# Kernel tuning notes

Measured on AMD Instinct MI355X. Metric: run time of the kernel, lower is better.

Reference implementation:

```python
import jax, jax.numpy as jnp
import numpy as np

N_EXPERTS = 8
DIM = 2048
INTER = 1408
TOTAL_TOKENS = 16384
ALPHA = 1.702
LIMIT = 7.0
LINEAR_OFFSET = 1.0


def setup_inputs() -> dict:
    key = jax.random.key(0)
    k1, k2, k3, k4 = jax.random.split(key, 4)
    x = jax.random.normal(k1, (TOTAL_TOKENS, DIM), dtype=jnp.float32)
    permuted_probs = jax.random.uniform(k2, (TOTAL_TOKENS, 1), dtype=jnp.float32)
    # Stacked-transposed views as in gate_and_up_projs / down_projs properties:
    # [E, in_features, out_features]
    gate_up_w = jax.random.normal(k3, (N_EXPERTS, DIM, 2 * INTER), dtype=jnp.float32) * (DIM ** -0.5)
    down_w = jax.random.normal(k4, (N_EXPERTS, INTER, DIM), dtype=jnp.float32) * (INTER ** -0.5)
    tokens_per_expert = jnp.full((N_EXPERTS,), TOTAL_TOKENS // N_EXPERTS, dtype=jnp.int32)
    return {"x": x, "permuted_probs": permuted_probs, "gate_up_w": gate_up_w,
            "down_w": down_w, "tokens_per_expert": tokens_per_expert}


def quick_geglu(h, probs):
    # interleaved split, as x[..., ::2] / x[..., 1::2]
    gate = jnp.minimum(h[..., ::2], LIMIT)
    up = jnp.clip(h[..., 1::2], -LIMIT, LIMIT)
    glu = gate * jax.nn.sigmoid(ALPHA * gate)
    inter = glu * (up + LINEAR_OFFSET)
    return (inter * probs).astype(h.dtype)


def reference(x, permuted_probs, gate_up_w, down_w, tokens_per_expert):
    # tokens are pre-permuted: equal static group sizes per expert (fp8 pad/unpad
    # is an identity on the math; grouped GEMM expressed as batched einsum).
    E = gate_up_w.shape[0]
    xr = x.reshape(E, -1, DIM)                      # [E, T, dim]
    h = jnp.einsum('etd,edf->etf', xr, gate_up_w)   # [E, T, 2*inter]
    probs = permuted_probs.reshape(E, -1, 1)
    act = quick_geglu(h, probs)                     # [E, T, inter]
    out = jnp.einsum('eti,eio->eto', act, down_w)   # [E, T, dim]
    return out.reshape(-1, DIM)
```

## Files before the change

### kernel.cpp

```cpp
#include <hip/hip_runtime.h>
#include <hip/hip_bf16.h>
#include <stdint.h>

#define N_EXPERTS 8
#define DIM 2048
#define INTER 1408
#define NGU (2*INTER)
#define TOK_E 2048
#define TOTAL_TOKENS 16384

typedef __attribute__((ext_vector_type(8))) short short8;
typedef __attribute__((ext_vector_type(4))) float f32x4;

__device__ __forceinline__ unsigned short f2bf(float f) {
    union { float f; unsigned u; } v; v.f = f;
    unsigned r = v.u + 0x7FFF + ((v.u >> 16) & 1);
    return (unsigned short)(r >> 16);
}

#define GLOAD16(G, L) __builtin_amdgcn_global_load_lds( \
    (const __attribute__((address_space(1))) void*)(G), \
    (__attribute__((address_space(3))) void*)(L), 16, 0, 0)


__global__ void convert_x(const float* __restrict__ in, unsigned short* __restrict__ out, int n8) {
    int i = blockIdx.x * blockDim.x + threadIdx.x;
    int stride = gridDim.x * blockDim.x;
    for (; i < n8; i += stride) {
        const float4* p = (const float4*)(in + (size_t)i * 8);
        float4 v0 = p[0], v1 = p[1];
        union { unsigned short u[8]; uint4 q; } o;
        o.u[0]=f2bf(v0.x); o.u[1]=f2bf(v0.y); o.u[2]=f2bf(v0.z); o.u[3]=f2bf(v0.w);
        o.u[4]=f2bf(v1.x); o.u[5]=f2bf(v1.y); o.u[6]=f2bf(v1.z); o.u[7]=f2bf(v1.w);
        *(uint4*)(out + (size_t)i * 8) = o.q;
    }
}

__global__ __launch_bounds__(256)
void transpose_convert(const float* __restrict__ in, unsigned short* __restrict__ out,
                       int K, int N, int permute) {
    __shared__ float tile[32][129];
    const int n0 = blockIdx.x * 32, k0 = blockIdx.y * 128;
    const size_t ein  = (size_t)blockIdx.z * K * N;
    const size_t eout = (size_t)blockIdx.z * N * K;
    const int tc = threadIdx.x & 31;
    const int tr = threadIdx.x >> 5;
    #pragma unroll
    for (int i = 0; i < 16; ++i) {
        int k = tr + i * 8;
        tile[tc][k] = in[ein + (size_t)(k0 + k) * N + n0 + tc];
    }
    __syncthreads();
    const int kg = threadIdx.x & 31;
    const int r0 = threadIdx.x >> 5;
    #pragma unroll
    for (int i = 0; i < 4; ++i) {
        int r = r0 + i * 8;
        int c = n0 + r;
        int dr = c;
        if (permute) {
            int a = c >> 1;
            dr = ((a >> 4) << 5) + (a & 15) + ((c & 1) << 4);
        }
        union { unsigned short u[4]; uint2 q; } o;
        #pragma unroll
        for (int j = 0; j < 4; ++j) o.u[j] = f2bf(tile[r][kg * 4 + j]);
        *(uint2*)(out + eout + (size_t)dr * K + k0 + kg * 4) = o.q;
    }
}


#define SB0 __builtin_amdgcn_sched_barrier(0)
#define VMC(N_) asm volatile("s_waitcnt vmcnt(" #N_ ")" ::: "memory")
#define LGK8 asm volatile("s_waitcnt lgkmcnt(8)" ::: "memory")

#define GEMM_PROLOG(LDKC) \
    const int t = threadIdx.x; \
    const int lane = t & 63, wid = t >> 6; \
    const int wm = wid >> 2, wn = wid & 3;             \
    const int l15 = lane & 15; \
    const int rd0 = (lane & 15) * 64 + (((lane >> 4) ^ (lane & 7)) * 8); \
    const int rd1 = (lane & 15) * 64 + ((((lane >> 4) + 4) ^ (lane & 7)) * 8); \
    const size_t goff = (size_t)(t >> 3) * (LDKC) + (size_t)(((t & 7) ^ ((t >> 3) & 7)) * 8); \
    const int ldsw = wid * 512 + lane * 8;

#define STGA(LDKC, bb_, h_, kt_) do { \
    const unsigned short* g_ = gA + (size_t)(h_) * 128 * (LDKC) + (size_t)(kt_) * 64 + goff; \
    unsigned short* l_ = sA + (bb_) * 16384 + (h_) * 8192 + ldsw; \
    GLOAD16(g_, l_); GLOAD16(g_ + (size_t)64 * (LDKC), l_ + 4096); \
} while (0)

#define STGB(LDKC, bb_, h_, kt_) do { \
    const unsigned short* g_ = gB + (size_t)(h_) * 128 * (LDKC) + (size_t)(kt_) * 64 + goff; \
    unsigned short* l_ = sB + (bb_) * 16384 + (h_) * 8192 + ldsw; \
    GLOAD16(g_, l_); GLOAD16(g_ + (size_t)64 * (LDKC), l_ + 4096); \
} while (0)

#define DSA2(bb_, qm_) do { \
    const unsigned short* p_ = &sA[(bb_) * 16384 + ((qm_) * 128 + wm * 64) * 64]; \
    _Pragma("unroll") for (int m_ = 0; m_ < 4; ++m_) { \
        a[m_][0] = *(const short8*)(p_ + m_ * 1024 + rd0); \
        a[m_][1] = *(const short8*)(p_ + m_ * 1024 + rd1); } \
} while (0)

#define DSB2(bb_, qn_, R_) do { \
    const unsigned short* p_ = &sB[(bb_) * 16384 + ((qn_) * 128 + wn * 32) * 64]; \
    _Pragma("unroll") for (int n_ = 0; n_ < 2; ++n_) { \
        R_[n_][0] = *(const short8*)(p_ + n_ * 1024 + rd0); \
        R_[n_][1] = *(const short8*)(p_ + n_ * 1024 + rd1); } \
} while (0)

#define QMF(qm_, qn_, B_) do { \
    _Pragma("unroll") for (int m_ = 0; m_ < 4; ++m_) { \
        _Pragma("unroll") for (int n_ = 0; n_ < 2; ++n_) { \
            acc[qm_][qn_][m_][n_] = __builtin_amdgcn_mfma_f32_16x16x32_bf16(a[m_][0], B_[n_][0], acc[qm_][qn_][m_][n_], 0, 0, 0); \
            acc[qm_][qn_][m_][n_] = __builtin_amdgcn_mfma_f32_16x16x32_bf16(a[m_][1], B_[n_][1], acc[qm_][qn_][m_][n_], 0, 0, 0); \
        } } \
} while (0)

#define PH(DSOPS, STGOPS, MFOPS, ENDOPS) do { \
    DSOPS; \
    STGOPS; \
    SB0; \
    __builtin_amdgcn_s_barrier(); \
    asm volatile("s_waitcnt lgkmcnt(0)" ::: "memory"); \
    SB0; \
    __builtin_amdgcn_s_setprio(1); \
    MFOPS; \
    __builtin_amdgcn_s_setprio(0); \
    SB0; \
    ENDOPS; \
    __builtin_amdgcn_s_barrier(); \
} while (0)

#define ITER8(LDKC, kt0_, SG2, SG3, SG4, SG5, SG6, SG7, SG8, E4, E8) \
    PH(DSA2(0,0); DSB2(0,0,bq0); LGK8, STGA(LDKC,1,1,(kt0_)+1), QMF(0,0,bq0), ); \
    PH(DSB2(0,1,bq1),            SG2,                     QMF(0,1,bq1), ); \
    PH(DSA2(0,1),                SG3,                     QMF(1,0,bq0), ); \
    PH(,                         SG4,                     QMF(1,1,bq1), E4); \
    PH(DSA2(1,0); DSB2(1,0,bq0); LGK8, SG5,               QMF(0,0,bq0), ); \
    PH(DSB2(1,1,bq1),            SG6,                     QMF(0,1,bq1), ); \
    PH(DSA2(1,1),                SG7,                     QMF(1,0,bq0), ); \
    PH(,                         SG8,                     QMF(1,1,bq1), E8);

#define GEMM_PIPE(LDKC, NI_) \
    short8 a[4][2], bq0[2][2], bq1[2][2]; \
    f32x4 acc[2][2][4][2]; \
    _Pragma("unroll") for (int q_ = 0; q_ < 2; ++q_) \
    _Pragma("unroll") for (int r_ = 0; r_ < 2; ++r_) \
    _Pragma("unroll") for (int m_ = 0; m_ < 4; ++m_) \
    _Pragma("unroll") for (int n_ = 0; n_ < 2; ++n_) acc[q_][r_][m_][n_] = (f32x4)0.0f; \
     \
    STGA(LDKC,0,0,0); STGB(LDKC,0,0,0); STGB(LDKC,0,1,0); STGA(LDKC,0,1,0); \
    STGA(LDKC,1,0,1); STGB(LDKC,1,0,1); STGB(LDKC,1,1,1); \
    VMC(6); \
    __builtin_amdgcn_s_barrier(); \
    for (int it = 0; it < (NI_) - 1; ++it) { \
        const int kt0 = 2 * it; \
        ITER8(LDKC, kt0, \
              STGA(LDKC,0,0,kt0+2), STGB(LDKC,0,0,kt0+2), STGB(LDKC,0,1,kt0+2), STGA(LDKC,0,1,kt0+2), \
              STGA(LDKC,1,0,kt0+3), STGB(LDKC,1,0,kt0+3), STGB(LDKC,1,1,kt0+3), \
              VMC(6), VMC(6)) \
    } \
    { \
        const int kt0 = 2 * ((NI_) - 1); \
        ITER8(LDKC, kt0, , , , , , , , VMC(0), ) \
    }


__global__ __launch_bounds__(512, 2)
void gemm_gu(const unsigned short* __restrict__ A,
             const unsigned short* __restrict__ Bt,
             const float* __restrict__ probs,
             unsigned short* __restrict__ act) {
    __shared__ unsigned short sA[2 * 16384];
    __shared__ unsigned short sB[2 * 16384];
    GEMM_PROLOG(DIM)
    const int bid = blockIdx.x;
    const int e = bid & 7;
    const int local = bid >> 3;
    const int tm = local & 7;
    const int tn = local >> 3;
    const unsigned short* gA = A  + (size_t)(e * TOK_E + tm * 256) * DIM;
    const unsigned short* gB = Bt + (size_t)e * NGU * DIM + (size_t)(tn * 256) * DIM;

    GEMM_PIPE(DIM, 16)

    const int rgrp = lane >> 4;
    #pragma unroll
    for (int qm = 0; qm < 2; ++qm) {
        #pragma unroll
        for (int qn = 0; qn < 2; ++qn) {
            const int acol = tn * 128 + qn * 64 + wn * 16 + l15;
            #pragma unroll
            for (int m = 0; m < 4; ++m) {
                const int row0 = e * TOK_E + tm * 256 + qm * 128 + wm * 64 + m * 16 + rgrp * 4;
                #pragma unroll
                for (int j = 0; j < 4; ++j) {
                    float p = probs[row0 + j];
                    float g = fminf(acc[qm][qn][m][0][j], 7.0f);
                    float u = fminf(fmaxf(acc[qm][qn][m][1][j], -7.0f), 7.0f);
                    float glu = g / (1.0f + __expf(-1.702f * g));
                    float r = glu * (u + 1.0f) * p;
                    act[(size_t)(row0 + j) * INTER + acol] = f2bf(r);
                }
            }
        }
    }
}


__global__ __launch_bounds__(512, 2)
void gemm_down(const unsigned short* __restrict__ A,
               const unsigned short* __restrict__ Bt,
               float* __restrict__ out) {
    __shared__ unsigned short sA[2 * 16384];
    __shared__ unsigned short sB[2 * 16384];
    GEMM_PROLOG(INTER)
    const int bid = blockIdx.x;
    const int e = bid & 7;
    const int local = bid >> 3;
    const int tm = local & 7;
    const int tn = local >> 3;
    const unsigned short* gA = A  + (size_t)(e * TOK_E + tm * 256) * INTER;
    const unsigned short* gB = Bt + (size_t)e * DIM * INTER + (size_t)(tn * 256) * INTER;

    GEMM_PIPE(INTER, 11)

    const int rgrp = lane >> 4;
    #pragma unroll
    for (int qm = 0; qm < 2; ++qm) {
        #pragma unroll
        for (int qn = 0; qn < 2; ++qn) {
            #pragma unroll
            for (int m = 0; m < 4; ++m) {
                const int row0 = e * TOK_E + tm * 256 + qm * 128 + wm * 64 + m * 16 + rgrp * 4;
                #pragma unroll
                for (int j = 0; j < 4; ++j) {
                    #pragma unroll
                    for (int n = 0; n < 2; ++n) {
                        const int col = tn * 256 + qn * 128 + wn * 32 + n * 16 + l15;
                        out[(size_t)(row0 + j) * DIM + col] = acc[qm][qn][m][n][j];
                    }
                }
            }
        }
    }
}


extern "C" void kernel_launch(void* const* d_in, const int* in_sizes, int n_in,
                              void* d_out, int out_size, void* d_ws, size_t ws_size,
                              hipStream_t stream) {
    const float* x     = (const float*)d_in[0];
    const float* probs = (const float*)d_in[1];
    const float* gup   = (const float*)d_in[2];
    const float* dwn   = (const float*)d_in[3];
    float* out = (float*)d_out;

    char* ws = (char*)d_ws;
    const size_t SZ_XB  = (size_t)TOTAL_TOKENS * DIM * 2;
    const size_t SZ_GUB = (size_t)N_EXPERTS * NGU * DIM * 2;
    const size_t SZ_DWB = (size_t)N_EXPERTS * DIM * INTER * 2;
    unsigned short* xb   = (unsigned short*)(ws);
    unsigned short* gub  = (unsigned short*)(ws + SZ_XB);
    unsigned short* dwb  = (unsigned short*)(ws + SZ_XB + SZ_GUB);
    unsigned short* actb = (unsigned short*)(ws + SZ_XB + SZ_GUB + SZ_DWB);

    convert_x<<<2048, 256, 0, stream>>>(x, xb, TOTAL_TOKENS * DIM / 8);

    dim3 tg1(NGU / 32, DIM / 128, N_EXPERTS);
    transpose_convert<<<tg1, 256, 0, stream>>>(gup, gub, DIM, NGU, 1);
    dim3 tg2(DIM / 32, INTER / 128, N_EXPERTS);
    transpose_convert<<<tg2, 256, 0, stream>>>(dwn, dwb, INTER, DIM, 0);

    gemm_gu<<<704, 512, 0, stream>>>(xb, gub, probs, actb);
    gemm_down<<<512, 512, 0, stream>>>(actb, dwb, out);
}
```

Baseline: 407.6 us.

## Fuse the prep conversion kernels into one launch and drop explicit LDS waits

```diff
diff --git a/kernel.cpp b/kernel.cpp
--- a/kernel.cpp
+++ b/kernel.cpp
@@ -22,27 +22,46 @@
     (const __attribute__((address_space(1))) void*)(G), \
     (__attribute__((address_space(3))) void*)(L), 16, 0, 0)
 
-
-__global__ void convert_x(const float* __restrict__ in, unsigned short* __restrict__ out, int n8) {
-    int i = blockIdx.x * blockDim.x + threadIdx.x;
-    int stride = gridDim.x * blockDim.x;
-    for (; i < n8; i += stride) {
-        const float4* p = (const float4*)(in + (size_t)i * 8);
-        float4 v0 = p[0], v1 = p[1];
-        union { unsigned short u[8]; uint4 q; } o;
-        o.u[0]=f2bf(v0.x); o.u[1]=f2bf(v0.y); o.u[2]=f2bf(v0.z); o.u[3]=f2bf(v0.w);
-        o.u[4]=f2bf(v1.x); o.u[5]=f2bf(v1.y); o.u[6]=f2bf(v1.z); o.u[7]=f2bf(v1.w);
-        *(uint4*)(out + (size_t)i * 8) = o.q;
-    }
-}
+#define NB_CONV 2048
+#define NB_GUP  (88 * 16 * 8)
+#define NB_DWN  (64 * 11 * 8)
 
 __global__ __launch_bounds__(256)
-void transpose_convert(const float* __restrict__ in, unsigned short* __restrict__ out,
-                       int K, int N, int permute) {
+void prep_fused(const float* __restrict__ x, unsigned short* __restrict__ xb,
+                const float* __restrict__ gup, unsigned short* __restrict__ gub,
+                const float* __restrict__ dwn, unsigned short* __restrict__ dwb) {
     __shared__ float tile[32][129];
-    const int n0 = blockIdx.x * 32, k0 = blockIdx.y * 128;
-    const size_t ein  = (size_t)blockIdx.z * K * N;
-    const size_t eout = (size_t)blockIdx.z * N * K;
+    const int b = blockIdx.x;
+    if (b < NB_CONV) {
+        const int n8 = TOTAL_TOKENS * DIM / 8;
+        int i = b * 256 + threadIdx.x;
+        const int stride = NB_CONV * 256;
+        for (; i < n8; i += stride) {
+            const float4* p = (const float4*)(x + (size_t)i * 8);
+            float4 v0 = p[0], v1 = p[1];
+            union { unsigned short u[8]; uint4 q; } o;
+            o.u[0]=f2bf(v0.x); o.u[1]=f2bf(v0.y); o.u[2]=f2bf(v0.z); o.u[3]=f2bf(v0.w);
+            o.u[4]=f2bf(v1.x); o.u[5]=f2bf(v1.y); o.u[6]=f2bf(v1.z); o.u[7]=f2bf(v1.w);
+            *(uint4*)(xb + (size_t)i * 8) = o.q;
+        }
+        return;
+    }
+    const float* in; unsigned short* out; int K, N, permute, local, nbx;
+    if (b < NB_CONV + NB_GUP) {
+        in = gup; out = gub; K = DIM; N = NGU; permute = 1;
+        local = b - NB_CONV; nbx = NGU / 32;
+    } else {
+        in = dwn; out = dwb; K = INTER; N = DIM; permute = 0;
+        local = b - NB_CONV - NB_GUP; nbx = DIM / 32;
+    }
+    const int bx = local % nbx;
+    const int rem = local / nbx;
+    const int nby = K / 128;
+    const int by = rem % nby;
+    const int bz = rem / nby;
+    const int n0 = bx * 32, k0 = by * 128;
+    const size_t ein  = (size_t)bz * K * N;
+    const size_t eout = (size_t)bz * N * K;
     const int tc = threadIdx.x & 31;
     const int tr = threadIdx.x >> 5;
     #pragma unroll
@@ -72,7 +91,6 @@
 
 #define SB0 __builtin_amdgcn_sched_barrier(0)
 #define VMC(N_) asm volatile("s_waitcnt vmcnt(" #N_ ")" ::: "memory")
-#define LGK8 asm volatile("s_waitcnt lgkmcnt(8)" ::: "memory")
 
 #define GEMM_PROLOG(LDKC) \
     const int t = threadIdx.x; \
@@ -123,8 +141,6 @@
     STGOPS; \
     SB0; \
     __builtin_amdgcn_s_barrier(); \
-    asm volatile("s_waitcnt lgkmcnt(0)" ::: "memory"); \
-    SB0; \
     __builtin_amdgcn_s_setprio(1); \
     MFOPS; \
     __builtin_amdgcn_s_setprio(0); \
@@ -134,11 +150,11 @@
 } while (0)
 
 #define ITER8(LDKC, kt0_, SG2, SG3, SG4, SG5, SG6, SG7, SG8, E4, E8) \
-    PH(DSA2(0,0); DSB2(0,0,bq0); LGK8, STGA(LDKC,1,1,(kt0_)+1), QMF(0,0,bq0), ); \
+    PH(DSA2(0,0); DSB2(0,0,bq0), STGA(LDKC,1,1,(kt0_)+1), QMF(0,0,bq0), ); \
     PH(DSB2(0,1,bq1),            SG2,                     QMF(0,1,bq1), ); \
     PH(DSA2(0,1),                SG3,                     QMF(1,0,bq0), ); \
     PH(,                         SG4,                     QMF(1,1,bq1), E4); \
-    PH(DSA2(1,0); DSB2(1,0,bq0); LGK8, SG5,               QMF(0,0,bq0), ); \
+    PH(DSA2(1,0); DSB2(1,0,bq0), SG5,                     QMF(0,0,bq0), ); \
     PH(DSB2(1,1,bq1),            SG6,                     QMF(0,1,bq1), ); \
     PH(DSA2(1,1),                SG7,                     QMF(1,0,bq0), ); \
     PH(,                         SG8,                     QMF(1,1,bq1), E8);
@@ -267,12 +283,7 @@
     unsigned short* dwb  = (unsigned short*)(ws + SZ_XB + SZ_GUB);
     unsigned short* actb = (unsigned short*)(ws + SZ_XB + SZ_GUB + SZ_DWB);
 
-    convert_x<<<2048, 256, 0, stream>>>(x, xb, TOTAL_TOKENS * DIM / 8);
-
-    dim3 tg1(NGU / 32, DIM / 128, N_EXPERTS);
-    transpose_convert<<<tg1, 256, 0, stream>>>(gup, gub, DIM, NGU, 1);
-    dim3 tg2(DIM / 32, INTER / 128, N_EXPERTS);
-    transpose_convert<<<tg2, 256, 0, stream>>>(dwn, dwb, INTER, DIM, 0);
+    prep_fused<<<NB_CONV + NB_GUP + NB_DWN, 256, 0, stream>>>(x, xb, gup, gub, dwn, dwb);
 
     gemm_gu<<<704, 512, 0, stream>>>(xb, gub, probs, actb);
     gemm_down<<<512, 512, 0, stream>>>(actb, dwb, out);
```

Measured after the change: 426.9 us. +4.7%, slower.

## Switch GEMMs to 32x32x16 MFMA with matching weight permutation and LDS reads

Applied to the files above, without the earlier changes.

```diff
diff --git a/kernel.cpp b/kernel.cpp
--- a/kernel.cpp
+++ b/kernel.cpp
@@ -10,7 +10,7 @@
 #define TOTAL_TOKENS 16384
 
 typedef __attribute__((ext_vector_type(8))) short short8;
-typedef __attribute__((ext_vector_type(4))) float f32x4;
+typedef __attribute__((ext_vector_type(16))) float f32x16;
 
 __device__ __forceinline__ unsigned short f2bf(float f) {
     union { float f; unsigned u; } v; v.f = f;
@@ -60,7 +60,7 @@
         int dr = c;
         if (permute) {
             int a = c >> 1;
-            dr = ((a >> 4) << 5) + (a & 15) + ((c & 1) << 4);
+            dr = ((a >> 5) << 6) + (a & 31) + ((c & 1) << 5);
         }
         union { unsigned short u[4]; uint2 q; } o;
         #pragma unroll
@@ -78,9 +78,11 @@
     const int t = threadIdx.x; \
     const int lane = t & 63, wid = t >> 6; \
     const int wm = wid >> 2, wn = wid & 3;             \
-    const int l15 = lane & 15; \
-    const int rd0 = (lane & 15) * 64 + (((lane >> 4) ^ (lane & 7)) * 8); \
-    const int rd1 = (lane & 15) * 64 + ((((lane >> 4) + 4) ^ (lane & 7)) * 8); \
+    const int row31 = lane & 31, h5 = lane >> 5; \
+    const int so0 = ((0 * 2 + h5) ^ (lane & 7)) * 8; \
+    const int so1 = ((1 * 2 + h5) ^ (lane & 7)) * 8; \
+    const int so2 = ((2 * 2 + h5) ^ (lane & 7)) * 8; \
+    const int so3 = ((3 * 2 + h5) ^ (lane & 7)) * 8; \
     const size_t goff = (size_t)(t >> 3) * (LDKC) + (size_t)(((t & 7) ^ ((t >> 3) & 7)) * 8); \
     const int ldsw = wid * 512 + lane * 8;
 
@@ -97,24 +99,23 @@
 } while (0)
 
 #define DSA2(bb_, qm_) do { \
-    const unsigned short* p_ = &sA[(bb_) * 16384 + ((qm_) * 128 + wm * 64) * 64]; \
-    _Pragma("unroll") for (int m_ = 0; m_ < 4; ++m_) { \
-        a[m_][0] = *(const short8*)(p_ + m_ * 1024 + rd0); \
-        a[m_][1] = *(const short8*)(p_ + m_ * 1024 + rd1); } \
+    const unsigned short* p_ = &sA[(bb_) * 16384 + ((qm_) * 128 + wm * 64 + row31) * 64]; \
+    a[0][0] = *(const short8*)(p_ + so0);        a[0][1] = *(const short8*)(p_ + so1); \
+    a[0][2] = *(const short8*)(p_ + so2);        a[0][3] = *(const short8*)(p_ + so3); \
+    a[1][0] = *(const short8*)(p_ + 2048 + so0); a[1][1] = *(const short8*)(p_ + 2048 + so1); \
+    a[1][2] = *(const short8*)(p_ + 2048 + so2); a[1][3] = *(const short8*)(p_ + 2048 + so3); \
 } while (0)
 
 #define DSB2(bb_, qn_, R_) do { \
-    const unsigned short* p_ = &sB[(bb_) * 16384 + ((qn_) * 128 + wn * 32) * 64]; \
-    _Pragma("unroll") for (int n_ = 0; n_ < 2; ++n_) { \
-        R_[n_][0] = *(const short8*)(p_ + n_ * 1024 + rd0); \
-        R_[n_][1] = *(const short8*)(p_ + n_ * 1024 + rd1); } \
+    const unsigned short* p_ = &sB[(bb_) * 16384 + (wn * 64 + (qn_) * 32 + row31) * 64]; \
+    R_[0] = *(const short8*)(p_ + so0); R_[1] = *(const short8*)(p_ + so1); \
+    R_[2] = *(const short8*)(p_ + so2); R_[3] = *(const short8*)(p_ + so3); \
 } while (0)
 
 #define QMF(qm_, qn_, B_) do { \
-    _Pragma("unroll") for (int m_ = 0; m_ < 4; ++m_) { \
-        _Pragma("unroll") for (int n_ = 0; n_ < 2; ++n_) { \
-            acc[qm_][qn_][m_][n_] = __builtin_amdgcn_mfma_f32_16x16x32_bf16(a[m_][0], B_[n_][0], acc[qm_][qn_][m_][n_], 0, 0, 0); \
-            acc[qm_][qn_][m_][n_] = __builtin_amdgcn_mfma_f32_16x16x32_bf16(a[m_][1], B_[n_][1], acc[qm_][qn_][m_][n_], 0, 0, 0); \
+    _Pragma("unroll") for (int s_ = 0; s_ < 4; ++s_) { \
+        _Pragma("unroll") for (int m_ = 0; m_ < 2; ++m_) { \
+            acc[qm_][qn_][m_] = __builtin_amdgcn_mfma_f32_32x32x16_bf16(a[m_][s_], B_[s_], acc[qm_][qn_][m_], 0, 0, 0); \
         } } \
 } while (0)
 
@@ -122,15 +123,14 @@
     DSOPS; \
     STGOPS; \
     SB0; \
+    asm volatile("s_waitcnt lgkmcnt(0)" ::: "memory"); \
+    ENDOPS; \
+    SB0; \
     __builtin_amdgcn_s_barrier(); \
-    asm volatile("s_waitcnt lgkmcnt(0)" ::: "memory"); \
-    SB0; \
     __builtin_amdgcn_s_setprio(1); \
     MFOPS; \
     __builtin_amdgcn_s_setprio(0); \
     SB0; \
-    ENDOPS; \
-    __builtin_amdgcn_s_barrier(); \
 } while (0)
 
 #define ITER8(LDKC, kt0_, SG2, SG3, SG4, SG5, SG6, SG7, SG8, E4, E8) \
@@ -144,12 +144,11 @@
     PH(,                         SG8,                     QMF(1,1,bq1), E8);
 
 #define GEMM_PIPE(LDKC, NI_) \
-    short8 a[4][2], bq0[2][2], bq1[2][2]; \
-    f32x4 acc[2][2][4][2]; \
+    short8 a[2][4], bq0[4], bq1[4]; \
+    f32x16 acc[2][2][2]; \
     _Pragma("unroll") for (int q_ = 0; q_ < 2; ++q_) \
     _Pragma("unroll") for (int r_ = 0; r_ < 2; ++r_) \
-    _Pragma("unroll") for (int m_ = 0; m_ < 4; ++m_) \
-    _Pragma("unroll") for (int n_ = 0; n_ < 2; ++n_) acc[q_][r_][m_][n_] = (f32x4)0.0f; \
+    _Pragma("unroll") for (int m_ = 0; m_ < 2; ++m_) acc[q_][r_][m_] = (f32x16)0.0f; \
      \
     STGA(LDKC,0,0,0); STGB(LDKC,0,0,0); STGB(LDKC,0,1,0); STGA(LDKC,0,1,0); \
     STGA(LDKC,1,0,1); STGB(LDKC,1,0,1); STGB(LDKC,1,1,1); \
@@ -186,24 +185,21 @@
 
     GEMM_PIPE(DIM, 16)
 
-    const int rgrp = lane >> 4;
+    const int acol = tn * 128 + wn * 32 + row31;
     #pragma unroll
     for (int qm = 0; qm < 2; ++qm) {
         #pragma unroll
-        for (int qn = 0; qn < 2; ++qn) {
-            const int acol = tn * 128 + qn * 64 + wn * 16 + l15;
+        for (int m = 0; m < 2; ++m) {
+            const int rbase = e * TOK_E + tm * 256 + qm * 128 + wm * 64 + m * 32 + 4 * h5;
             #pragma unroll
-            for (int m = 0; m < 4; ++m) {
-                const int row0 = e * TOK_E + tm * 256 + qm * 128 + wm * 64 + m * 16 + rgrp * 4;
-                #pragma unroll
-                for (int j = 0; j < 4; ++j) {
-                    float p = probs[row0 + j];
-                    float g = fminf(acc[qm][qn][m][0][j], 7.0f);
-                    float u = fminf(fmaxf(acc[qm][qn][m][1][j], -7.0f), 7.0f);
-                    float glu = g / (1.0f + __expf(-1.702f * g));
-                    float r = glu * (u + 1.0f) * p;
-                    act[(size_t)(row0 + j) * INTER + acol] = f2bf(r);
-                }
+            for (int r = 0; r < 16; ++r) {
+                const int row = rbase + (r & 3) + 8 * (r >> 2);
+                float p = probs[row];
+                float g = fminf(acc[qm][0][m][r], 7.0f);
+                float u = fminf(fmaxf(acc[qm][1][m][r], -7.0f), 7.0f);
+                float glu = g / (1.0f + __expf(-1.702f * g));
+                float rv = glu * (u + 1.0f) * p;
+                act[(size_t)row * INTER + acol] = f2bf(rv);
             }
         }
     }
@@ -227,21 +223,18 @@
 
     GEMM_PIPE(INTER, 11)
 
-    const int rgrp = lane >> 4;
     #pragma unroll
     for (int qm = 0; qm < 2; ++qm) {
         #pragma unroll
         for (int qn = 0; qn < 2; ++qn) {
+            const int col = tn * 256 + wn * 64 + qn * 32 + row31;
             #pragma unroll
-            for (int m = 0; m < 4; ++m) {
-                const int row0 = e * TOK_E + tm * 256 + qm * 128 + wm * 64 + m * 16 + rgrp * 4;
+            for (int m = 0; m < 2; ++m) {
+                const int rbase = e * TOK_E + tm * 256 + qm * 128 + wm * 64 + m * 32 + 4 * h5;
                 #pragma unroll
-                for (int j = 0; j < 4; ++j) {
-                    #pragma unroll
-                    for (int n = 0; n < 2; ++n) {
-                        const int col = tn * 256 + qn * 128 + wn * 32 + n * 16 + l15;
-                        out[(size_t)(row0 + j) * DIM + col] = acc[qm][qn][m][n][j];
-                    }
+                for (int r = 0; r < 16; ++r) {
+                    const int row = rbase + (r & 3) + 8 * (r >> 2);
+                    out[(size_t)row * DIM + col] = acc[qm][qn][m][r];
                 }
             }
         }
```

Result: slower. 470.7 us (+15.5%).
